# Optimization experiments

Hardware: AMD Instinct MI355X
Metric: run time of the kernel (lower is better)

## Reference

```python
import jax, jax.numpy as jnp
import numpy as np

DIM = 512
D_IN = 4096
N_OBJ = 2048
N_REL = 32768
STEPS = 2
N_OBJ_CLS = 151
N_REL_CLS = 51
EPS = 1e-5


def _mlp2(x, w1, b1, w2, b2):
    # Linear -> ReLU -> Linear (torch Linear: y = x W^T + b)
    return jnp.maximum(x @ w1.T + b1, 0.0) @ w2.T + b2


def _gate(a, b, w, bias):
    # Sequential(Linear(2*dim, 1), Sigmoid) on cat([a, b], 1)
    return jax.nn.sigmoid(jnp.concatenate([a, b], axis=1) @ w.T + bias)


def _gru_cell(x, h, wih, whh, bih, bhh):
    gi = x @ wih.T + bih  # [N, 3*DIM]
    gh = h @ whh.T + bhh
    ir, iz, inew = jnp.split(gi, 3, axis=1)
    hr, hz, hnew = jnp.split(gh, 3, axis=1)
    r = jax.nn.sigmoid(ir + hr)
    z = jax.nn.sigmoid(iz + hz)
    n = jnp.tanh(inew + r * hnew)
    return (1.0 - z) * n + z * h


def setup_inputs() -> dict:
    key = jax.random.key(0)
    ks = jax.random.split(key, 32)
    rn = lambda k, shape, s=0.02: jax.random.normal(k, shape, dtype=jnp.float32) * s
    z = lambda *shape: jnp.zeros(shape, dtype=jnp.float32)
    return {
        'x_obj': jax.random.normal(ks[0], (N_OBJ, D_IN), dtype=jnp.float32),
        'x_pred': jax.random.normal(ks[1], (N_REL, D_IN), dtype=jnp.float32),
        'rel_inds': jax.random.randint(ks[2], (N_REL, 2), 0, N_OBJ),
        # obj / pred embedding MLPs
        'oe_w1': rn(ks[3], (DIM, D_IN)), 'oe_b1': z(DIM),
        'oe_w2': rn(ks[4], (DIM, DIM)), 'oe_b2': z(DIM),
        'pe_w1': rn(ks[5], (DIM, D_IN)), 'pe_b1': z(DIM),
        'pe_w2': rn(ks[6], (DIM, DIM)), 'pe_b2': z(DIM),
        # gates: Linear(2*dim, 1)
        'g_sn_w': rn(ks[7], (1, 2 * DIM)), 'g_sn_b': z(1),
        'g_on_w': rn(ks[8], (1, 2 * DIM)), 'g_on_b': z(1),
        'g_se_w': rn(ks[9], (1, 2 * DIM)), 'g_se_b': z(1),
        'g_oe_w': rn(ks[10], (1, 2 * DIM)), 'g_oe_b': z(1),
        # GRU cells
        'ngru_wih': rn(ks[11], (3 * DIM, DIM)), 'ngru_whh': rn(ks[12], (3 * DIM, DIM)),
        'ngru_bih': z(3 * DIM), 'ngru_bhh': z(3 * DIM),
        'egru_wih': rn(ks[13], (3 * DIM, DIM)), 'egru_whh': rn(ks[14], (3 * DIM, DIM)),
        'egru_bih': z(3 * DIM), 'egru_bhh': z(3 * DIM),
        # classifier heads
        'op_w': rn(ks[15], (N_OBJ_CLS, DIM)), 'op_b': z(N_OBJ_CLS),
        'pp_w': rn(ks[16], (N_REL_CLS, DIM)), 'pp_b': z(N_REL_CLS),
    }


def reference(x_obj, x_pred, rel_inds,
              oe_w1, oe_b1, oe_w2, oe_b2,
              pe_w1, pe_b1, pe_w2, pe_b2,
              g_sn_w, g_sn_b, g_on_w, g_on_b,
              g_se_w, g_se_b, g_oe_w, g_oe_b,
              ngru_wih, ngru_whh, ngru_bih, ngru_bhh,
              egru_wih, egru_whh, egru_bih, egru_bhh,
              op_w, op_b, pp_w, pp_b):
    n_obj = x_obj.shape[0]
    subj_idx = rel_inds[:, 0]
    obj_idx = rel_inds[:, 1]

    h_obj = _mlp2(x_obj, oe_w1, oe_b1, oe_w2, oe_b2)    # [N_obj, DIM]
    h_edge = _mlp2(x_pred, pe_w1, pe_b1, pe_w2, pe_b2)  # [N_rel, DIM]

    # row sums of the 0/1 subj/obj_pred_map == in-degree counts (constants)
    ones = jnp.ones((rel_inds.shape[0],), dtype=jnp.float32)
    cnt_s = jax.ops.segment_sum(ones, subj_idx, num_segments=n_obj)[:, None]
    cnt_o = jax.ops.segment_sum(ones, obj_idx, num_segments=n_obj)[:, None]

    for _ in range(STEPS):
        sub_vert = h_obj[subj_idx]  # [N_rel, DIM]
        obj_vert = h_obj[obj_idx]

        # node update: gated edge->node messages, mean-aggregated per node
        msg_p2s = _gate(sub_vert, h_edge, g_sn_w, g_sn_b) * h_edge
        msg_p2o = _gate(obj_vert, h_edge, g_on_w, g_on_b) * h_edge
        node_message = (
            jax.ops.segment_sum(msg_p2s, subj_idx, num_segments=n_obj) / (cnt_s + EPS)
            + jax.ops.segment_sum(msg_p2o, obj_idx, num_segments=n_obj) / (cnt_o + EPS)
        ) / 2.0
        new_h_obj = _gru_cell(node_message, h_obj, ngru_wih, ngru_whh, ngru_bih, ngru_bhh)

        # edge update: gated node->edge messages
        msg_s2p = _gate(sub_vert, h_edge, g_se_w, g_se_b) * sub_vert
        msg_o2p = _gate(obj_vert, h_edge, g_oe_w, g_oe_b) * obj_vert
        edge_message = (msg_s2p + msg_o2p) / 2.0
        h_edge = _gru_cell(edge_message, h_edge, egru_wih, egru_whh, egru_bih, egru_bhh)
        h_obj = new_h_obj

    obj_class_logits = h_obj @ op_w.T + op_b    # [N_obj, 151]
    pred_class_logits = h_edge @ pp_w.T + pp_b  # [N_rel, 51]
    obj_class_labels = jnp.argmax(obj_class_logits[:, 1:], axis=1) + 1
    return (h_obj, h_edge, obj_class_logits, pred_class_logits, obj_class_labels, rel_inds)
```

## Files before the change

### kernel.cpp

```cpp
#include <hip/hip_runtime.h>
#include <math.h>

typedef unsigned short u16;
typedef unsigned int u32;
typedef _Float16 f16;
typedef f16 f16x8 __attribute__((ext_vector_type(8)));
typedef float f32x4 __attribute__((ext_vector_type(4)));

#define DIM 512
#define D_IN 4096
#define N_OBJS 2048
#define N_RELS 32768
#define N_OBJ_CLS 151
#define N_REL_CLS 51
#define EPSV 1e-5f

#define OFF_HOBJ  0
#define OFF_HEDGE (N_OBJS*DIM)
#define OFF_OLOG  (OFF_HEDGE + N_RELS*DIM)
#define OFF_PLOG  (OFF_OLOG + N_OBJS*N_OBJ_CLS)
#define OFF_LBL   (OFF_PLOG + N_RELS*N_REL_CLS)
#define OFF_RI    (OFF_LBL + N_OBJS)

__device__ __forceinline__ float sigmoidf_(float x) { return 1.0f / (1.0f + expf(-x)); }
__device__ __forceinline__ u16 f2h_(float f) {
    union { f16 h; u16 u; } c; c.h = (f16)f; return c.u;
}
__device__ __forceinline__ float h2f_(u16 u) {
    union { f16 h; u16 u; } c; c.u = u; return (float)c.h;
}

__device__ __forceinline__ void cvt8h1(const float* f, uint4& h) {
    u32 hh[8];
#pragma unroll
    for (int i = 0; i < 8; i++) hh[i] = f2h_(f[i]);
    h.x = hh[0] | (hh[1] << 16); h.y = hh[2] | (hh[3] << 16);
    h.z = hh[4] | (hh[5] << 16); h.w = hh[6] | (hh[7] << 16);
}
__device__ __forceinline__ void cvt8h2(const float* f, uint4& h, uint4& l) {
    u32 hh[8], ll[8];
#pragma unroll
    for (int i = 0; i < 8; i++) {
        u16 x = f2h_(f[i]);
        hh[i] = x;
        ll[i] = f2h_(f[i] - h2f_(x));
    }
    h.x = hh[0] | (hh[1] << 16); h.y = hh[2] | (hh[3] << 16);
    h.z = hh[4] | (hh[5] << 16); h.w = hh[6] | (hh[7] << 16);
    l.x = ll[0] | (ll[1] << 16); l.y = ll[2] | (ll[3] << 16);
    l.z = ll[4] | (ll[5] << 16); l.w = ll[6] | (ll[7] << 16);
}

__device__ __forceinline__ int swzo(int row, int c) {
    return row * 32 + ((c ^ ((row >> 1) & 3)) << 3);
}

__device__ __forceinline__ int xcdswz(int orig, int nwg) {
    const int q = nwg >> 3;
    return (orig & 7) * q + (orig >> 3);
}

__device__ __forceinline__ void gload16(const void* g, void* l) {
    __builtin_amdgcn_global_load_lds(
        (const __attribute__((address_space(1))) void*)g,
        (__attribute__((address_space(3))) void*)l, 16, 0, 0);
}

#define Q_BIG  (DIM * D_IN / 4)
#define Q_SQ   (DIM * DIM / 4)
#define Q_GRU  (3 * DIM * DIM / 4)
#define Q_OP   (N_OBJ_CLS * DIM / 4)
#define Q_PP   (N_REL_CLS * DIM / 4)
#define CV_C0  (Q_BIG)
#define CV_C1  (CV_C0 + Q_BIG)
#define CV_C2  (CV_C1 + Q_SQ)
#define CV_C3  (CV_C2 + Q_SQ)
#define CV_C4  (CV_C3 + Q_GRU)
#define CV_C5  (CV_C4 + Q_GRU)
#define CV_C6  (CV_C5 + Q_GRU)
#define CV_C7  (CV_C6 + Q_GRU)
#define CV_C8  (CV_C7 + Q_OP)
#define CV_C9  (CV_C8 + Q_PP)

__global__ __launch_bounds__(256) void convert_all(
    const float* __restrict__ s0, u16* __restrict__ d0,
    const float* __restrict__ s1, u16* __restrict__ d1,
    const float* __restrict__ s2, u16* __restrict__ d2,
    const float* __restrict__ s3, u16* __restrict__ d3,
    const float* __restrict__ s4, u16* __restrict__ d4,
    const float* __restrict__ s5, u16* __restrict__ d5,
    const float* __restrict__ s6, u16* __restrict__ d6,
    const float* __restrict__ s7, u16* __restrict__ d7,
    const float* __restrict__ s8, u16* __restrict__ d8,
    const float* __restrict__ s9, u16* __restrict__ d9)
{
    int i = blockIdx.x * 256 + threadIdx.x;
    if (i >= CV_C9) return;
    const float* src; u16* dst; int base;
    if      (i < CV_C0) { src = s0; dst = d0; base = 0; }
    else if (i < CV_C1) { src = s1; dst = d1; base = CV_C0; }
    else if (i < CV_C2) { src = s2; dst = d2; base = CV_C1; }
    else if (i < CV_C3) { src = s3; dst = d3; base = CV_C2; }
    else if (i < CV_C4) { src = s4; dst = d4; base = CV_C3; }
    else if (i < CV_C5) { src = s5; dst = d5; base = CV_C4; }
    else if (i < CV_C6) { src = s6; dst = d6; base = CV_C5; }
    else if (i < CV_C7) { src = s7; dst = d7; base = CV_C6; }
    else if (i < CV_C8) { src = s8; dst = d8; base = CV_C7; }
    else                { src = s9; dst = d9; base = CV_C8; }
    const int q = i - base;
    const float4 v = ((const float4*)src)[q];
    ((ushort4*)dst)[q] = make_ushort4(f2h_(v.x), f2h_(v.y), f2h_(v.z), f2h_(v.w));
}

template<bool RELU, int AT, bool WSPLIT>
__device__ __forceinline__ void gemm_a32_body(
    int id, u16* sAh, u16* sBh, u16* sAl,
    const float* __restrict__ A, const u16* __restrict__ Bhi,
    const float* __restrict__ bias, u16* __restrict__ Chi, u16* __restrict__ Clo,
    int NX, int K)
{
    const int m0 = (id / NX) * 128, n0 = (id % NX) * 128;
    const int N = NX * 128;
    const int t = threadIdx.x;
    const int wid = t >> 6, lane = t & 63;
    const int wm = (wid >> 1) * 64, wn = (wid & 1) * 64;
    const int lr = lane & 15, lk = lane >> 4;

    f32x4 acc[4][4] = {};

    const int sr = t >> 1;
    const int sc = (t & 1) * 2;
    const float* Ap = A + (size_t)(m0 + sr) * K + (t & 1) * 16;

    const int rB = (wid * 2) * 16 + (lane >> 2);
    const int cB = (lane & 3) ^ ((rB >> 1) & 3);
    const u16* Bp0 = Bhi + (size_t)(n0 + rB) * K + cB * 8;
    const u16* Bp1 = Bp0 + (size_t)16 * K;
    u16* Bd0 = &sBh[(wid * 2) * 512];
    u16* Bd1 = Bd0 + 512;

    float fv[16];
    *(float4*)&fv[0]  = *(const float4*)(Ap);
    *(float4*)&fv[4]  = *(const float4*)(Ap + 4);
    *(float4*)&fv[8]  = *(const float4*)(Ap + 8);
    *(float4*)&fv[12] = *(const float4*)(Ap + 12);

    for (int k0 = 0; k0 < K; k0 += 32) {
        uint4 ah0, ah1, al0, al1;
        if (AT == 2) { cvt8h2(fv, ah0, al0); cvt8h2(fv + 8, ah1, al1); }
        else         { cvt8h1(fv, ah0);      cvt8h1(fv + 8, ah1); }

        __syncthreads();
        gload16(Bp0 + k0, Bd0);
        gload16(Bp1 + k0, Bd1);
        *(uint4*)&sAh[swzo(sr, sc)]     = ah0;
        *(uint4*)&sAh[swzo(sr, sc + 1)] = ah1;
        if (AT == 2) {
            *(uint4*)&sAl[swzo(sr, sc)]     = al0;
            *(uint4*)&sAl[swzo(sr, sc + 1)] = al1;
        }
        asm volatile("s_waitcnt vmcnt(0)" ::: "memory");
        __syncthreads();

        const int kn = k0 + 32;
        if (kn < K) {
            *(float4*)&fv[0]  = *(const float4*)(Ap + kn);
            *(float4*)&fv[4]  = *(const float4*)(Ap + kn + 4);
            *(float4*)&fv[8]  = *(const float4*)(Ap + kn + 8);
            *(float4*)&fv[12] = *(const float4*)(Ap + kn + 12);
        }

        f16x8 ah[4], al[4], bh[4];
#pragma unroll
        for (int f = 0; f < 4; f++) {
            const int off = swzo(wm + f * 16 + lr, lk);
            ah[f] = *(const f16x8*)&sAh[off];
            if (AT == 2) al[f] = *(const f16x8*)&sAl[off];
            bh[f] = *(const f16x8*)&sBh[swzo(wn + f * 16 + lr, lk)];
        }
#pragma unroll
        for (int fm = 0; fm < 4; fm++)
#pragma unroll
            for (int fn = 0; fn < 4; fn++) {
                acc[fm][fn] = __builtin_amdgcn_mfma_f32_16x16x32_f16(ah[fm], bh[fn], acc[fm][fn], 0, 0, 0);
                if (AT == 2)
                    acc[fm][fn] = __builtin_amdgcn_mfma_f32_16x16x32_f16(al[fm], bh[fn], acc[fm][fn], 0, 0, 0);
            }
    }
#pragma unroll
    for (int fm = 0; fm < 4; fm++) {
        const int mrow = m0 + wm + fm * 16 + lk * 4;
#pragma unroll
        for (int fn = 0; fn < 4; fn++) {
            const int col = n0 + wn + fn * 16 + lr;
            const float bv = bias[col];
#pragma unroll
            for (int j = 0; j < 4; j++) {
                float v = acc[fm][fn][j] + bv;
                if (RELU) v = fmaxf(v, 0.0f);
                const u16 h = f2h_(v);
                Chi[(size_t)(mrow + j) * N + col] = h;
                if (WSPLIT) Clo[(size_t)(mrow + j) * N + col] = f2h_(v - h2f_(h));
            }
        }
    }
}

__global__ __launch_bounds__(256, 3) void enc1_both(
    const float* __restrict__ xp, const u16* __restrict__ pw,
    const float* __restrict__ pb, u16* __restrict__ tmpe,
    const float* __restrict__ xo, const u16* __restrict__ ow,
    const float* __restrict__ ob, u16* __restrict__ tmpoh, u16* __restrict__ tmpol)
{
    __shared__ u16 smem[3 * 4096];
    const int id = xcdswz(blockIdx.x, gridDim.x);
    if (id < 1024)
        gemm_a32_body<true, 1, false>(id, smem, smem + 4096, nullptr,
                                      xp, pw, pb, tmpe, nullptr, 4, D_IN);
    else
        gemm_a32_body<true, 2, true>(id - 1024, smem, smem + 4096, smem + 8192,
                                     xo, ow, ob, tmpoh, tmpol, 4, D_IN);
}

template<int AT, bool WF32, bool WHI, bool WLO>
__device__ __forceinline__ void gemm_f16_body(
    int id, u16* smem,
    const u16* __restrict__ Ahi, const u16* __restrict__ Alo,
    const u16* __restrict__ Bhi, const float* __restrict__ bias,
    float* __restrict__ C32, u16* __restrict__ Chi, u16* __restrict__ Clo,
    int NX, int N, int ldc, int K)
{
    const int m0 = (id / NX) * 128, n0 = (id % NX) * 128;
    const int t = threadIdx.x;
    const int wid = t >> 6, lane = t & 63;
    const int wm = (wid >> 1) * 64, wn = (wid & 1) * 64;
    const int lr = lane & 15, lk = lane >> 4;

    f32x4 acc[4][4] = {};

    const int rr = (wid * 2) * 16 + (lane >> 2);
    const int cc = (lane & 3) ^ ((rr >> 1) & 3);
    const u16* pA0 = Ahi + (size_t)(m0 + rr) * K + cc * 8;
    const u16* pA1 = pA0 + (size_t)16 * K;
    const u16* pL0 = (AT == 2) ? Alo + (size_t)(m0 + rr) * K + cc * 8 : nullptr;
    const u16* pL1 = (AT == 2) ? pL0 + (size_t)16 * K : nullptr;
    const u16* pB0 = Bhi + (size_t)(n0 + rr) * K + cc * 8;
    const u16* pB1 = pB0 + (size_t)16 * K;
    const int bOff = (wid * 2) * 512;

    for (int k0 = 0; k0 < K; k0 += 64) {
        __syncthreads();
#pragma unroll
        for (int h = 0; h < 2; h++) {
            const int kk = k0 + h * 32;
            u16* sA_ = smem + h * 4096;
            u16* sB_ = smem + 8192 + h * 4096;
            gload16(pA0 + kk, sA_ + bOff);
            gload16(pA1 + kk, sA_ + bOff + 512);
            if (AT == 2) {
                u16* sL_ = smem + 16384 + h * 4096;
                gload16(pL0 + kk, sL_ + bOff);
                gload16(pL1 + kk, sL_ + bOff + 512);
            }
            gload16(pB0 + kk, sB_ + bOff);
            gload16(pB1 + kk, sB_ + bOff + 512);
        }
        asm volatile("s_waitcnt vmcnt(0)" ::: "memory");
        __syncthreads();

#pragma unroll
        for (int h = 0; h < 2; h++) {
            const u16* sA_ = smem + h * 4096;
            const u16* sB_ = smem + 8192 + h * 4096;
            const u16* sL_ = smem + 16384 + h * 4096;
            f16x8 ah[4], al[4], bh[4];
#pragma unroll
            for (int f = 0; f < 4; f++) {
                const int off = swzo(wm + f * 16 + lr, lk);
                ah[f] = *(const f16x8*)&sA_[off];
                if (AT == 2) al[f] = *(const f16x8*)&sL_[off];
                bh[f] = *(const f16x8*)&sB_[swzo(wn + f * 16 + lr, lk)];
            }
#pragma unroll
            for (int fm = 0; fm < 4; fm++)
#pragma unroll
                for (int fn = 0; fn < 4; fn++) {
                    acc[fm][fn] = __builtin_amdgcn_mfma_f32_16x16x32_f16(ah[fm], bh[fn], acc[fm][fn], 0, 0, 0);
                    if (AT == 2)
                        acc[fm][fn] = __builtin_amdgcn_mfma_f32_16x16x32_f16(al[fm], bh[fn], acc[fm][fn], 0, 0, 0);
                }
        }
    }
#pragma unroll
    for (int fm = 0; fm < 4; fm++) {
        const int mrow = m0 + wm + fm * 16 + lk * 4;
#pragma unroll
        for (int fn = 0; fn < 4; fn++) {
            const int col = n0 + wn + fn * 16 + lr;
            const float bv = bias[col];
#pragma unroll
            for (int j = 0; j < 4; j++) {
                const float v = acc[fm][fn][j] + bv;
                if (WF32 && col < N) C32[(size_t)(mrow + j) * ldc + col] = v;
                if (WHI) {
                    const u16 h = f2h_(v);
                    Chi[(size_t)(mrow + j) * (NX * 128) + col] = h;
                    if (WLO)
                        Clo[(size_t)(mrow + j) * (NX * 128) + col] = f2h_(v - h2f_(h));
                }
            }
        }
    }
}

template<int AT, bool WF32, bool WHI, bool WLO>
__global__ __launch_bounds__(256, AT == 1 ? 4 : 3) void gemm_f16(
    const u16* __restrict__ Ahi, const u16* __restrict__ Alo,
    const u16* __restrict__ Bhi, const float* __restrict__ bias,
    float* __restrict__ C32, u16* __restrict__ Chi, u16* __restrict__ Clo,
    int NX, int N, int ldc, int K)
{
    __shared__ u16 smem[AT == 2 ? 6 * 4096 : 4 * 4096];
    const int id = xcdswz(blockIdx.x, gridDim.x);
    gemm_f16_body<AT, WF32, WHI, WLO>(id, smem, Ahi, Alo, Bhi, bias,
                                      C32, Chi, Clo, NX, N, ldc, K);
}

__global__ __launch_bounds__(256, 3) void cls_both(
    const u16* __restrict__ hhe, const u16* __restrict__ pph,
    const float* __restrict__ ppb, float* __restrict__ plog,
    const u16* __restrict__ hhoh, const u16* __restrict__ hhol,
    const u16* __restrict__ oph, const float* __restrict__ opb,
    float* __restrict__ olog)
{
    __shared__ u16 smem[6 * 4096];
    const int id = xcdswz(blockIdx.x, gridDim.x);
    if (id < 256)
        gemm_f16_body<1, true, false, false>(id, smem, hhe, nullptr, pph, ppb,
                                             plog, nullptr, nullptr,
                                             1, N_REL_CLS, N_REL_CLS, DIM);
    else
        gemm_f16_body<2, true, false, false>(id - 256, smem, hhoh, hhol, oph, opb,
                                             olog, nullptr, nullptr,
                                             2, N_OBJ_CLS, N_OBJ_CLS, DIM);
}

__global__ __launch_bounds__(256, 4) void gru_gemm_e(
    const u16* __restrict__ Xh, const u16* __restrict__ WiH,
    const float* __restrict__ bi, u16* __restrict__ gi,
    const u16* __restrict__ Hh, const u16* __restrict__ WhH,
    const float* __restrict__ bhs, u16* __restrict__ gh_)
{
    __shared__ u16 smem[4 * 4096];
    const int id = xcdswz(blockIdx.x, gridDim.x);
    const int part = id % 24;
    const int m0b = id / 24;
    const bool isH = part >= 12;
    const int nblk = part - (isH ? 12 : 0);
    gemm_f16_body<1, false, true, false>(m0b * 12 + nblk, smem,
        isH ? Hh : Xh, nullptr, isH ? WhH : WiH, isH ? bhs : bi,
        nullptr, isH ? gh_ : gi, nullptr, 12, 1536, 1536, DIM);
}

__global__ __launch_bounds__(256, 3) void gru_edge_obj(
    const u16* __restrict__ Xe, const u16* __restrict__ WeI,
    const float* __restrict__ beI, u16* __restrict__ geI,
    const u16* __restrict__ He, const u16* __restrict__ WeH,
    const float* __restrict__ beH, u16* __restrict__ geH,
    int nEdge,
    const u16* __restrict__ Xoh, const u16* __restrict__ Xol,
    const u16* __restrict__ WoI, const float* __restrict__ boI, u16* __restrict__ goI,
    const u16* __restrict__ Hoh, const u16* __restrict__ Hol,
    const u16* __restrict__ WoH, const float* __restrict__ boH, u16* __restrict__ goH)
{
    __shared__ u16 smem[6 * 4096];
    const int id = xcdswz(blockIdx.x, gridDim.x);
    if (id < nEdge) {
        const int part = id % 24;
        const int m0b = id / 24;
        const bool isH = part >= 12;
        const int nblk = part - (isH ? 12 : 0);
        gemm_f16_body<1, false, true, false>(m0b * 12 + nblk, smem,
            isH ? He : Xe, nullptr, isH ? WeH : WeI, isH ? beH : beI,
            nullptr, isH ? geH : geI, nullptr, 12, 1536, 1536, DIM);
    } else {
        const int oid = id - nEdge;
        const int part = oid % 24;
        const int m0b = oid / 24;
        const bool isH = part >= 12;
        const int nblk = part - (isH ? 12 : 0);
        gemm_f16_body<2, false, true, false>(m0b * 12 + nblk, smem,
            isH ? Hoh : Xoh, isH ? Hol : Xol, isH ? WoH : WoI, isH ? boH : boI,
            nullptr, isH ? goH : goI, nullptr, 12, 1536, 1536, DIM);
    }
}

__device__ __forceinline__ float gcomb(u16 ir, u16 iz, u16 in_, u16 hr, u16 hz,
                                       u16 hn, float h) {
    const float r = sigmoidf_(h2f_(ir) + h2f_(hr));
    const float z = sigmoidf_(h2f_(iz) + h2f_(hz));
    const float n = tanhf(h2f_(in_) + r * h2f_(hn));
    return (1.0f - z) * n + z * h;
}

template<bool WSPLIT, bool WF32>
__global__ __launch_bounds__(256) void gru_combine(
    const u16* __restrict__ gi, const u16* __restrict__ gh,
    u16* __restrict__ hh, u16* __restrict__ hl, float* __restrict__ H32, int R)
{
    const int idx = blockIdx.x * 256 + threadIdx.x;
    if (idx >= R * 128) return;
    const int r = idx >> 7, c4 = (idx & 127) * 4;
    const size_t gb = (size_t)r * 1536 + c4;
    const ushort4 ir4 = *(const ushort4*)&gi[gb];
    const ushort4 iz4 = *(const ushort4*)&gi[gb + 512];
    const ushort4 in4 = *(const ushort4*)&gi[gb + 1024];
    const ushort4 hr4 = *(const ushort4*)&gh[gb];
    const ushort4 hz4 = *(const ushort4*)&gh[gb + 512];
    const ushort4 hn4 = *(const ushort4*)&gh[gb + 1024];
    const size_t hb = (size_t)r * 512 + c4;
    const ushort4 hhi = *(const ushort4*)&hh[hb];
    float h0 = h2f_(hhi.x), h1 = h2f_(hhi.y), h2 = h2f_(hhi.z), h3 = h2f_(hhi.w);
    if (WSPLIT) {
        const ushort4 hlo = *(const ushort4*)&hl[hb];
        h0 += h2f_(hlo.x); h1 += h2f_(hlo.y); h2 += h2f_(hlo.z); h3 += h2f_(hlo.w);
    }
    float4 o;
    o.x = gcomb(ir4.x, iz4.x, in4.x, hr4.x, hz4.x, hn4.x, h0);
    o.y = gcomb(ir4.y, iz4.y, in4.y, hr4.y, hz4.y, hn4.y, h1);
    o.z = gcomb(ir4.z, iz4.z, in4.z, hr4.z, hz4.z, hn4.z, h2);
    o.w = gcomb(ir4.w, iz4.w, in4.w, hr4.w, hz4.w, hn4.w, h3);
    const ushort4 hi4 = make_ushort4(f2h_(o.x), f2h_(o.y), f2h_(o.z), f2h_(o.w));
    *(ushort4*)&hh[hb] = hi4;
    if (WSPLIT) {
        *(ushort4*)&hl[hb] = make_ushort4(
            f2h_(o.x - h2f_(hi4.x)), f2h_(o.y - h2f_(hi4.y)),
            f2h_(o.z - h2f_(hi4.z)), f2h_(o.w - h2f_(hi4.w)));
    }
    if (WF32) *(float4*)&H32[hb] = o;
}

__global__ __launch_bounds__(256) void count_int(const int* __restrict__ rel,
                                                 int* cs, int* co)
{
    const int e = blockIdx.x * 256 + threadIdx.x;
    atomicAdd(&cs[rel[2 * e]], 1);
    atomicAdd(&co[rel[2 * e + 1]], 1);
}

__global__ __launch_bounds__(256) void scan_off(const int* __restrict__ cs,
    const int* __restrict__ co, int* __restrict__ offs, int* __restrict__ offo)
{
    __shared__ int tmp[256];
    for (int arr = 0; arr < 2; arr++) {
        const int* c = arr ? co : cs;
        int* off = arr ? offo : offs;
        const int base = threadIdx.x * 8;
        int loc[8]; int s = 0;
#pragma unroll
        for (int j = 0; j < 8; j++) { loc[j] = c[base + j]; s += loc[j]; }
        tmp[threadIdx.x] = s;
        __syncthreads();
        for (int d = 1; d < 256; d <<= 1) {
            const int v = (threadIdx.x >= d) ? tmp[threadIdx.x - d] : 0;
            __syncthreads();
            tmp[threadIdx.x] += v;
            __syncthreads();
        }
        int p = tmp[threadIdx.x] - s;
#pragma unroll
        for (int j = 0; j < 8; j++) { off[base + j] = p; p += loc[j]; }
        __syncthreads();
    }
}

__global__ __launch_bounds__(256) void fill_csr(const int* __restrict__ rel,
    int* curS, int* curO, const int* __restrict__ offs, const int* __restrict__ offo,
    int* __restrict__ listS, int* __restrict__ listO)
{
    const int e = blockIdx.x * 256 + threadIdx.x;
    const int s = rel[2 * e], o = rel[2 * e + 1];
    const int i = atomicAdd(&curS[s], 1);
    listS[offs[s] + i] = e;
    const int j = atomicAdd(&curO[o], 1);
    listO[offo[o] + j] = e;
}

__global__ __launch_bounds__(256) void gatepass(
    const u16* __restrict__ hho, const u16* __restrict__ hhe,
    const int* __restrict__ rel,
    const float* __restrict__ wsn, const float* __restrict__ bsn,
    const float* __restrict__ won, const float* __restrict__ bon,
    const float* __restrict__ wse, const float* __restrict__ bse,
    const float* __restrict__ woe, const float* __restrict__ boe,
    const int* __restrict__ cs, const int* __restrict__ co,
    u16* __restrict__ emh, float* __restrict__ af, float* __restrict__ ag)
{
    const int e = blockIdx.x * 4 + (threadIdx.x >> 6);
    const int lane = threadIdx.x & 63;
    const int s = rel[2 * e], o = rel[2 * e + 1];
    const int c = lane * 8;

    const uint4 hsu = *(const uint4*)&hho[(size_t)s * DIM + c];
    const uint4 hou = *(const uint4*)&hho[(size_t)o * DIM + c];
    const uint4 heu = *(const uint4*)&hhe[(size_t)e * DIM + c];
    float hs[8], ho[8], he[8];
    hs[0] = h2f_((u16)hsu.x); hs[1] = h2f_((u16)(hsu.x >> 16));
    hs[2] = h2f_((u16)hsu.y); hs[3] = h2f_((u16)(hsu.y >> 16));
    hs[4] = h2f_((u16)hsu.z); hs[5] = h2f_((u16)(hsu.z >> 16));
    hs[6] = h2f_((u16)hsu.w); hs[7] = h2f_((u16)(hsu.w >> 16));
    ho[0] = h2f_((u16)hou.x); ho[1] = h2f_((u16)(hou.x >> 16));
    ho[2] = h2f_((u16)hou.y); ho[3] = h2f_((u16)(hou.y >> 16));
    ho[4] = h2f_((u16)hou.z); ho[5] = h2f_((u16)(hou.z >> 16));
    ho[6] = h2f_((u16)hou.w); ho[7] = h2f_((u16)(hou.w >> 16));
    he[0] = h2f_((u16)heu.x); he[1] = h2f_((u16)(heu.x >> 16));
    he[2] = h2f_((u16)heu.y); he[3] = h2f_((u16)(heu.y >> 16));
    he[4] = h2f_((u16)heu.z); he[5] = h2f_((u16)(heu.z >> 16));
    he[6] = h2f_((u16)heu.w); he[7] = h2f_((u16)(heu.w >> 16));

    float p0 = 0.f, p1 = 0.f, p2 = 0.f, p3 = 0.f;
#pragma unroll
    for (int q = 0; q < 2; q++) {
        const float4 w0v = *(const float4*)&wsn[c + q * 4];
        const float4 w0e = *(const float4*)&wsn[DIM + c + q * 4];
        const float4 w1v = *(const float4*)&won[c + q * 4];
        const float4 w1e = *(const float4*)&won[DIM + c + q * 4];
        const float4 w2v = *(const float4*)&wse[c + q * 4];
        const float4 w2e = *(const float4*)&wse[DIM + c + q * 4];
        const float4 w3v = *(const float4*)&woe[c + q * 4];
        const float4 w3e = *(const float4*)&woe[DIM + c + q * 4];
        const float* s4 = &hs[q * 4];
        const float* o4 = &ho[q * 4];
        const float* e4 = &he[q * 4];
        p0 += s4[0]*w0v.x + s4[1]*w0v.y + s4[2]*w0v.z + s4[3]*w0v.w
            + e4[0]*w0e.x + e4[1]*w0e.y + e4[2]*w0e.z + e4[3]*w0e.w;
        p1 += o4[0]*w1v.x + o4[1]*w1v.y + o4[2]*w1v.z + o4[3]*w1v.w
            + e4[0]*w1e.x + e4[1]*w1e.y + e4[2]*w1e.z + e4[3]*w1e.w;
        p2 += s4[0]*w2v.x + s4[1]*w2v.y + s4[2]*w2v.z + s4[3]*w2v.w
            + e4[0]*w2e.x + e4[1]*w2e.y + e4[2]*w2e.z + e4[3]*w2e.w;
        p3 += o4[0]*w3v.x + o4[1]*w3v.y + o4[2]*w3v.z + o4[3]*w3v.w
            + e4[0]*w3e.x + e4[1]*w3e.y + e4[2]*w3e.z + e4[3]*w3e.w;
    }
#pragma unroll
    for (int off = 32; off; off >>= 1) {
        p0 += __shfl_xor(p0, off);
        p1 += __shfl_xor(p1, off);
        p2 += __shfl_xor(p2, off);
        p3 += __shfl_xor(p3, off);
    }
    const float gsn = sigmoidf_(p0 + bsn[0]);
    const float gon = sigmoidf_(p1 + bon[0]);
    const float gse = sigmoidf_(p2 + bse[0]);
    const float goe = sigmoidf_(p3 + boe[0]);

    if (lane == 0) {
        af[e] = 0.5f * gsn / ((float)cs[s] + EPSV);
        ag[e] = 0.5f * gon / ((float)co[o] + EPSV);
    }
    u16 em8[8];
#pragma unroll
    for (int j = 0; j < 8; j++)
        em8[j] = f2h_(0.5f * (gse * hs[j] + goe * ho[j]));
    *(uint4*)&emh[(size_t)e * DIM + c] = *(const uint4*)em8;
}

__global__ __launch_bounds__(256) void gather_nm(
    const u16* __restrict__ hhe,
    const int* __restrict__ listS, const int* __restrict__ listO,
    const int* __restrict__ offs, const int* __restrict__ offo,
    const int* __restrict__ cs, const int* __restrict__ co,
    const float* __restrict__ af, const float* __restrict__ ag,
    u16* __restrict__ nmh, u16* __restrict__ nml)
{
    const int v = blockIdx.x * 4 + (threadIdx.x >> 6);
    const int lane = threadIdx.x & 63;
    const int c = lane * 8;

    float acc[8] = {};
#pragma unroll
    for (int side = 0; side < 2; side++) {
        const int* list = side ? listO : listS;
        const int b = side ? offo[v] : offs[v];
        const int n = side ? co[v] : cs[v];
        const float* coef = side ? ag : af;
        for (int i = 0; i < n; i++) {
            const int e = list[b + i];
            const float a = coef[e];
            const uint4 x = *(const uint4*)&hhe[(size_t)e * DIM + c];
            acc[0] += a * h2f_((u16)x.x); acc[1] += a * h2f_((u16)(x.x >> 16));
            acc[2] += a * h2f_((u16)x.y); acc[3] += a * h2f_((u16)(x.y >> 16));
            acc[4] += a * h2f_((u16)x.z); acc[5] += a * h2f_((u16)(x.z >> 16));
            acc[6] += a * h2f_((u16)x.w); acc[7] += a * h2f_((u16)(x.w >> 16));
        }
    }
    u16 hi8[8], lo8[8];
#pragma unroll
    for (int j = 0; j < 8; j++) {
        hi8[j] = f2h_(acc[j]);
        lo8[j] = f2h_(acc[j] - h2f_(hi8[j]));
    }
    *(uint4*)&nmh[(size_t)v * DIM + c] = *(const uint4*)hi8;
    *(uint4*)&nml[(size_t)v * DIM + c] = *(const uint4*)lo8;
}

__global__ __launch_bounds__(256) void argmax_kernel(const float* __restrict__ logits,
                                                     float* __restrict__ out)
{
    const int row = blockIdx.x * 4 + (threadIdx.x >> 6);
    const int lane = threadIdx.x & 63;
    float bv = -1e30f; int bi = 1;
    for (int j = 1 + lane; j < N_OBJ_CLS; j += 64) {
        const float v = logits[(size_t)row * N_OBJ_CLS + j];
        if (v > bv) { bv = v; bi = j; }
    }
#pragma unroll
    for (int off = 32; off; off >>= 1) {
        const float ov = __shfl_xor(bv, off);
        const int oi = __shfl_xor(bi, off);
        if (ov > bv || (ov == bv && oi < bi)) { bv = ov; bi = oi; }
    }
    if (lane == 0) out[row] = (float)bi;
}

__global__ __launch_bounds__(256) void relinds_kernel(const int* __restrict__ rel,
                                                      float* __restrict__ out)
{
    const int i = blockIdx.x * 256 + threadIdx.x;
    out[i] = (float)rel[i];
}

extern "C" void kernel_launch(void* const* d_in, const int* in_sizes, int n_in,
                              void* d_out, int out_size, void* d_ws, size_t ws_size,
                              hipStream_t stream)
{
    const float* x_obj = (const float*)d_in[0];
    const float* x_pred = (const float*)d_in[1];
    const int* rel = (const int*)d_in[2];
    const float* oe_w1 = (const float*)d_in[3];
    const float* oe_b1 = (const float*)d_in[4];
    const float* oe_w2 = (const float*)d_in[5];
    const float* oe_b2 = (const float*)d_in[6];
    const float* pe_w1 = (const float*)d_in[7];
    const float* pe_b1 = (const float*)d_in[8];
    const float* pe_w2 = (const float*)d_in[9];
    const float* pe_b2 = (const float*)d_in[10];
    const float* g_sn_w = (const float*)d_in[11];
    const float* g_sn_b = (const float*)d_in[12];
    const float* g_on_w = (const float*)d_in[13];
    const float* g_on_b = (const float*)d_in[14];
    const float* g_se_w = (const float*)d_in[15];
    const float* g_se_b = (const float*)d_in[16];
    const float* g_oe_w = (const float*)d_in[17];
    const float* g_oe_b = (const float*)d_in[18];
    const float* ngru_wih = (const float*)d_in[19];
    const float* ngru_whh = (const float*)d_in[20];
    const float* ngru_bih = (const float*)d_in[21];
    const float* ngru_bhh = (const float*)d_in[22];
    const float* egru_wih = (const float*)d_in[23];
    const float* egru_whh = (const float*)d_in[24];
    const float* egru_bih = (const float*)d_in[25];
    const float* egru_bhh = (const float*)d_in[26];
    const float* op_w = (const float*)d_in[27];
    const float* op_b = (const float*)d_in[28];
    const float* pp_w = (const float*)d_in[29];
    const float* pp_b = (const float*)d_in[30];

    float* out = (float*)d_out;

    float* h_obj = out + OFF_HOBJ;
    float* h_edge = out + OFF_HEDGE;

    char* wsp = (char*)d_ws;
    float* af = (float*)wsp; wsp += N_RELS * 4;
    float* ag = (float*)wsp; wsp += N_RELS * 4;
    int* cs = (int*)wsp;   wsp += N_OBJS * 4;
    int* co = (int*)wsp;   wsp += N_OBJS * 4;
    int* offs = (int*)wsp; wsp += N_OBJS * 4;
    int* offo = (int*)wsp; wsp += N_OBJS * 4;
    int* curS = (int*)wsp; wsp += N_OBJS * 4;
    int* curO = (int*)wsp; wsp += N_OBJS * 4;
    int* listS = (int*)wsp; wsp += N_RELS * 4;
    int* listO = (int*)wsp; wsp += N_RELS * 4;

    u16* wp = (u16*)wsp;
    const int s_big = DIM * D_IN, s_sq = DIM * DIM, s_gru = 3 * DIM * DIM;
    u16 *oe1h = wp; wp += s_big;
    u16 *pe1h = wp; wp += s_big;
    u16 *oe2h = wp; wp += s_sq;
    u16 *pe2h = wp; wp += s_sq;
    u16 *nih_h = wp; wp += s_gru;
    u16 *nhh_h = wp; wp += s_gru;
    u16 *eih_h = wp; wp += s_gru;
    u16 *ehh_h = wp; wp += s_gru;
    u16 *oph = wp; wp += 256 * DIM;
    u16 *pph = wp; wp += 128 * DIM;
    u16 *tmpo_h = wp; wp += (size_t)N_OBJS * DIM;
    u16 *tmpo_l = wp; wp += (size_t)N_OBJS * DIM;
    u16 *tmpe_h = wp; wp += (size_t)N_RELS * DIM;
    u16 *hhoh = wp; wp += (size_t)N_OBJS * DIM;
    u16 *hhol = wp; wp += (size_t)N_OBJS * DIM;
    u16 *hhe  = wp; wp += (size_t)N_RELS * DIM;
    u16 *emh  = wp; wp += (size_t)N_RELS * DIM;
    u16 *nmh  = wp; wp += (size_t)N_OBJS * DIM;
    u16 *nml  = wp; wp += (size_t)N_OBJS * DIM;
    u16 *gio = wp; wp += (size_t)N_OBJS * 1536;
    u16 *gho = wp; wp += (size_t)N_OBJS * 1536;

    const size_t used = (size_t)((char*)wp - (char*)d_ws);
    int R = 8192;
    if (used + (size_t)16384 * 6144 <= ws_size) R = 16384;
    u16* gi = wp;
    u16* gh = gi + (size_t)R * 1536;

    convert_all<<<(CV_C9 + 255) / 256, 256, 0, stream>>>(
        oe_w1, oe1h, pe_w1, pe1h, oe_w2, oe2h, pe_w2, pe2h,
        ngru_wih, nih_h, ngru_whh, nhh_h, egru_wih, eih_h, egru_whh, ehh_h,
        op_w, oph, pp_w, pph);

    hipMemsetAsync(cs, 0, 2 * N_OBJS * sizeof(int), stream);
    hipMemsetAsync(curS, 0, 2 * N_OBJS * sizeof(int), stream);
    count_int<<<N_RELS / 256, 256, 0, stream>>>(rel, cs, co);
    scan_off<<<1, 256, 0, stream>>>(cs, co, offs, offo);
    fill_csr<<<N_RELS / 256, 256, 0, stream>>>(rel, curS, curO, offs, offo, listS, listO);

    enc1_both<<<1088, 256, 0, stream>>>(
        x_pred, pe1h, pe_b1, tmpe_h,
        x_obj, oe1h, oe_b1, tmpo_h, tmpo_l);
    gemm_f16<1, false, true, false><<<4 * (N_RELS / 128), 256, 0, stream>>>(
        tmpe_h, nullptr, pe2h, pe_b2, nullptr, hhe, nullptr, 4, DIM, DIM, DIM);
    gemm_f16<2, false, true, true><<<4 * (N_OBJS / 128), 256, 0, stream>>>(
        tmpo_h, tmpo_l, oe2h, oe_b2, nullptr, hhoh, hhol, 4, DIM, DIM, DIM);

    for (int step = 0; step < 2; step++) {
        gatepass<<<N_RELS / 4, 256, 0, stream>>>(
            hhoh, hhe, rel,
            g_sn_w, g_sn_b, g_on_w, g_on_b, g_se_w, g_se_b, g_oe_w, g_oe_b,
            cs, co, emh, af, ag);
        gather_nm<<<N_OBJS / 4, 256, 0, stream>>>(
            hhe, listS, listO, offs, offo, cs, co, af, ag, nmh, nml);

        const int Rc0 = (N_RELS < R) ? N_RELS : R;
        const int nEdge = 24 * (Rc0 / 128);
        gru_edge_obj<<<nEdge + 24 * (N_OBJS / 128), 256, 0, stream>>>(
            emh, eih_h, egru_bih, gi, hhe, ehh_h, egru_bhh, gh, nEdge,
            nmh, nml, nih_h, ngru_bih, gio,
            hhoh, hhol, nhh_h, ngru_bhh, gho);

        if (step == 0)
            gru_combine<true, false><<<(N_OBJS * 128 + 255) / 256, 256, 0, stream>>>(
                gio, gho, hhoh, hhol, nullptr, N_OBJS);
        else
            gru_combine<true, true><<<(N_OBJS * 128 + 255) / 256, 256, 0, stream>>>(
                gio, gho, hhoh, hhol, h_obj, N_OBJS);
        if (step == 0)
            gru_combine<false, false><<<(Rc0 * 128 + 255) / 256, 256, 0, stream>>>(
                gi, gh, hhe, nullptr, nullptr, Rc0);
        else
            gru_combine<false, true><<<(Rc0 * 128 + 255) / 256, 256, 0, stream>>>(
                gi, gh, hhe, nullptr, h_edge, Rc0);

        for (int r0 = Rc0; r0 < N_RELS; r0 += R) {
            const int Rc = (N_RELS - r0 < R) ? (N_RELS - r0) : R;
            gru_gemm_e<<<24 * (Rc / 128), 256, 0, stream>>>(
                emh + (size_t)r0 * DIM, eih_h, egru_bih, gi,
                hhe + (size_t)r0 * DIM, ehh_h, egru_bhh, gh);
            if (step == 0)
                gru_combine<false, false><<<(Rc * 128 + 255) / 256, 256, 0, stream>>>(
                    gi, gh, hhe + (size_t)r0 * DIM, nullptr, nullptr, Rc);
            else
                gru_combine<false, true><<<(Rc * 128 + 255) / 256, 256, 0, stream>>>(
                    gi, gh, hhe + (size_t)r0 * DIM, nullptr, h_edge + (size_t)r0 * DIM, Rc);
        }
    }

    cls_both<<<288, 256, 0, stream>>>(
        hhe, pph, pp_b, out + OFF_PLOG,
        hhoh, hhol, oph, op_b, out + OFF_OLOG);

    argmax_kernel<<<N_OBJS / 4, 256, 0, stream>>>(out + OFF_OLOG, out + OFF_LBL);
    relinds_kernel<<<(2 * N_RELS) / 256, 256, 0, stream>>>(rel, out + OFF_RI);
}
```

Before: 1.031 ms.

## Split object GRU GEMM into separate hi/lo passes and fuse rel_inds output

The object-side GRU GEMM previously used a two-operand (hi+lo) split-precision body. It now runs as two independent single-operand GEMMs, one on the hi part and one on the lo part with a zero bias, writing separate hi/lo gate buffers. A new combine kernel sums these in fp32. This gives the combined edge+object kernel a uniform, lighter body, so it drops to 4-wave occupancy and a smaller shared-memory footprint. The rel_inds float copy moves into fill_csr, removing one launch. The cost is extra gate buffers and the memory traffic for them.

Result: faster. 982.3 us (median of 2 runs) (-4.7%).

```diff
diff --git a/kernel.cpp b/kernel.cpp
--- a/kernel.cpp
+++ b/kernel.cpp
@@ -362,18 +362,21 @@
         nullptr, isH ? gh_ : gi, nullptr, 12, 1536, 1536, DIM);
 }
 
-__global__ __launch_bounds__(256, 3) void gru_edge_obj(
+__global__ __launch_bounds__(256, 4) void gru_all1(
     const u16* __restrict__ Xe, const u16* __restrict__ WeI,
     const float* __restrict__ beI, u16* __restrict__ geI,
     const u16* __restrict__ He, const u16* __restrict__ WeH,
     const float* __restrict__ beH, u16* __restrict__ geH,
     int nEdge,
     const u16* __restrict__ Xoh, const u16* __restrict__ Xol,
-    const u16* __restrict__ WoI, const float* __restrict__ boI, u16* __restrict__ goI,
     const u16* __restrict__ Hoh, const u16* __restrict__ Hol,
-    const u16* __restrict__ WoH, const float* __restrict__ boH, u16* __restrict__ goH)
-{
-    __shared__ u16 smem[6 * 4096];
+    const u16* __restrict__ WoI, const u16* __restrict__ WoH,
+    const float* __restrict__ boI, const float* __restrict__ boH,
+    const float* __restrict__ zb,
+    u16* __restrict__ gioh, u16* __restrict__ giol,
+    u16* __restrict__ ghoh, u16* __restrict__ ghol)
+{
+    __shared__ u16 smem[4 * 4096];
     const int id = xcdswz(blockIdx.x, gridDim.x);
     if (id < nEdge) {
         const int part = id % 24;
@@ -383,30 +386,39 @@
         gemm_f16_body<1, false, true, false>(m0b * 12 + nblk, smem,
             isH ? He : Xe, nullptr, isH ? WeH : WeI, isH ? beH : beI,
             nullptr, isH ? geH : geI, nullptr, 12, 1536, 1536, DIM);
-    } else {
+    } else if (id < nEdge + 384) {
         const int oid = id - nEdge;
         const int part = oid % 24;
         const int m0b = oid / 24;
         const bool isH = part >= 12;
         const int nblk = part - (isH ? 12 : 0);
-        gemm_f16_body<2, false, true, false>(m0b * 12 + nblk, smem,
-            isH ? Hoh : Xoh, isH ? Hol : Xol, isH ? WoH : WoI, isH ? boH : boI,
-            nullptr, isH ? goH : goI, nullptr, 12, 1536, 1536, DIM);
-    }
-}
-
-__device__ __forceinline__ float gcomb(u16 ir, u16 iz, u16 in_, u16 hr, u16 hz,
-                                       u16 hn, float h) {
-    const float r = sigmoidf_(h2f_(ir) + h2f_(hr));
-    const float z = sigmoidf_(h2f_(iz) + h2f_(hz));
-    const float n = tanhf(h2f_(in_) + r * h2f_(hn));
+        gemm_f16_body<1, false, true, false>(m0b * 12 + nblk, smem,
+            isH ? Hoh : Xoh, nullptr, isH ? WoH : WoI, isH ? boH : boI,
+            nullptr, isH ? ghoh : gioh, nullptr, 12, 1536, 1536, DIM);
+    } else {
+        const int oid = id - nEdge - 384;
+        const int part = oid % 24;
+        const int m0b = oid / 24;
+        const bool isH = part >= 12;
+        const int nblk = part - (isH ? 12 : 0);
+        gemm_f16_body<1, false, true, false>(m0b * 12 + nblk, smem,
+            isH ? Hol : Xol, nullptr, isH ? WoH : WoI, zb,
+            nullptr, isH ? ghol : giol, nullptr, 12, 1536, 1536, DIM);
+    }
+}
+
+__device__ __forceinline__ float gcomb(float ir, float iz, float in_,
+                                       float hr, float hz, float hn, float h) {
+    const float r = sigmoidf_(ir + hr);
+    const float z = sigmoidf_(iz + hz);
+    const float n = tanhf(in_ + r * hn);
     return (1.0f - z) * n + z * h;
 }
 
-template<bool WSPLIT, bool WF32>
+template<bool WF32>
 __global__ __launch_bounds__(256) void gru_combine(
     const u16* __restrict__ gi, const u16* __restrict__ gh,
-    u16* __restrict__ hh, u16* __restrict__ hl, float* __restrict__ H32, int R)
+    u16* __restrict__ hh, float* __restrict__ H32, int R)
 {
     const int idx = blockIdx.x * 256 + threadIdx.x;
     if (idx >= R * 128) return;
@@ -420,24 +432,68 @@
     const ushort4 hn4 = *(const ushort4*)&gh[gb + 1024];
     const size_t hb = (size_t)r * 512 + c4;
     const ushort4 hhi = *(const ushort4*)&hh[hb];
-    float h0 = h2f_(hhi.x), h1 = h2f_(hhi.y), h2 = h2f_(hhi.z), h3 = h2f_(hhi.w);
-    if (WSPLIT) {
-        const ushort4 hlo = *(const ushort4*)&hl[hb];
-        h0 += h2f_(hlo.x); h1 += h2f_(hlo.y); h2 += h2f_(hlo.z); h3 += h2f_(hlo.w);
-    }
     float4 o;
-    o.x = gcomb(ir4.x, iz4.x, in4.x, hr4.x, hz4.x, hn4.x, h0);
-    o.y = gcomb(ir4.y, iz4.y, in4.y, hr4.y, hz4.y, hn4.y, h1);
-    o.z = gcomb(ir4.z, iz4.z, in4.z, hr4.z, hz4.z, hn4.z, h2);
-    o.w = gcomb(ir4.w, iz4.w, in4.w, hr4.w, hz4.w, hn4.w, h3);
-    const ushort4 hi4 = make_ushort4(f2h_(o.x), f2h_(o.y), f2h_(o.z), f2h_(o.w));
+    o.x = gcomb(h2f_(ir4.x), h2f_(iz4.x), h2f_(in4.x),
+                h2f_(hr4.x), h2f_(hz4.x), h2f_(hn4.x), h2f_(hhi.x));
+    o.y = gcomb(h2f_(ir4.y), h2f_(iz4.y), h2f_(in4.y),
+                h2f_(hr4.y), h2f_(hz4.y), h2f_(hn4.y), h2f_(hhi.y));
+    o.z = gcomb(h2f_(ir4.z), h2f_(iz4.z), h2f_(in4.z),
+                h2f_(hr4.z), h2f_(hz4.z), h2f_(hn4.z), h2f_(hhi.z));
+    o.w = gcomb(h2f_(ir4.w), h2f_(iz4.w), h2f_(in4.w),
+                h2f_(hr4.w), h2f_(hz4.w), h2f_(hn4.w), h2f_(hhi.w));
+    *(ushort4*)&hh[hb] = make_ushort4(f2h_(o.x), f2h_(o.y), f2h_(o.z), f2h_(o.w));
+    if (WF32) *(float4*)&H32[hb] = o;
+}
+
+template<bool WF32>
+__global__ __launch_bounds__(256) void gru_combine_o2(
+    const u16* __restrict__ gih, const u16* __restrict__ gil,
+    const u16* __restrict__ ghh_, const u16* __restrict__ ghl_,
+    u16* __restrict__ hh, u16* __restrict__ hl, float* __restrict__ H32, int R)
+{
+    const int idx = blockIdx.x * 256 + threadIdx.x;
+    if (idx >= R * 128) return;
+    const int r = idx >> 7, c4 = (idx & 127) * 4;
+    const size_t gb = (size_t)r * 1536 + c4;
+    ushort4 a, b;
+    float ir[4], iz[4], in_[4], hr[4], hz[4], hn[4];
+    a = *(const ushort4*)&gih[gb];        b = *(const ushort4*)&gil[gb];
+    ir[0] = h2f_(a.x) + h2f_(b.x); ir[1] = h2f_(a.y) + h2f_(b.y);
+    ir[2] = h2f_(a.z) + h2f_(b.z); ir[3] = h2f_(a.w) + h2f_(b.w);
+    a = *(const ushort4*)&gih[gb + 512];  b = *(const ushort4*)&gil[gb + 512];
+    iz[0] = h2f_(a.x) + h2f_(b.x); iz[1] = h2f_(a.y) + h2f_(b.y);
+    iz[2] = h2f_(a.z) + h2f_(b.z); iz[3] = h2f_(a.w) + h2f_(b.w);
+    a = *(const ushort4*)&gih[gb + 1024]; b = *(const ushort4*)&gil[gb + 1024];
+    in_[0] = h2f_(a.x) + h2f_(b.x); in_[1] = h2f_(a.y) + h2f_(b.y);
+    in_[2] = h2f_(a.z) + h2f_(b.z); in_[3] = h2f_(a.w) + h2f_(b.w);
+    a = *(const ushort4*)&ghh_[gb];        b = *(const ushort4*)&ghl_[gb];
+    hr[0] = h2f_(a.x) + h2f_(b.x); hr[1] = h2f_(a.y) + h2f_(b.y);
+    hr[2] = h2f_(a.z) + h2f_(b.z); hr[3] = h2f_(a.w) + h2f_(b.w);
+    a = *(const ushort4*)&ghh_[gb + 512];  b = *(const ushort4*)&ghl_[gb + 512];
+    hz[0] = h2f_(a.x) + h2f_(b.x); hz[1] = h2f_(a.y) + h2f_(b.y);
+    hz[2] = h2f_(a.z) + h2f_(b.z); hz[3] = h2f_(a.w) + h2f_(b.w);
+    a = *(const ushort4*)&ghh_[gb + 1024]; b = *(const ushort4*)&ghl_[gb + 1024];
+    hn[0] = h2f_(a.x) + h2f_(b.x); hn[1] = h2f_(a.y) + h2f_(b.y);
+    hn[2] = h2f_(a.z) + h2f_(b.z); hn[3] = h2f_(a.w) + h2f_(b.w);
+
+    const size_t hb = (size_t)r * 512 + c4;
+    const ushort4 hhi = *(const ushort4*)&hh[hb];
+    const ushort4 hlo = *(const ushort4*)&hl[hb];
+    float h[4];
+    h[0] = h2f_(hhi.x) + h2f_(hlo.x); h[1] = h2f_(hhi.y) + h2f_(hlo.y);
+    h[2] = h2f_(hhi.z) + h2f_(hlo.z); h[3] = h2f_(hhi.w) + h2f_(hlo.w);
+
+    float o[4];
+#pragma unroll
+    for (int j = 0; j < 4; j++)
+        o[j] = gcomb(ir[j], iz[j], in_[j], hr[j], hz[j], hn[j], h[j]);
+
+    const ushort4 hi4 = make_ushort4(f2h_(o[0]), f2h_(o[1]), f2h_(o[2]), f2h_(o[3]));
     *(ushort4*)&hh[hb] = hi4;
-    if (WSPLIT) {
-        *(ushort4*)&hl[hb] = make_ushort4(
-            f2h_(o.x - h2f_(hi4.x)), f2h_(o.y - h2f_(hi4.y)),
-            f2h_(o.z - h2f_(hi4.z)), f2h_(o.w - h2f_(hi4.w)));
-    }
-    if (WF32) *(float4*)&H32[hb] = o;
+    *(ushort4*)&hl[hb] = make_ushort4(
+        f2h_(o[0] - h2f_(hi4.x)), f2h_(o[1] - h2f_(hi4.y)),
+        f2h_(o[2] - h2f_(hi4.z)), f2h_(o[3] - h2f_(hi4.w)));
+    if (WF32) *(float4*)&H32[hb] = make_float4(o[0], o[1], o[2], o[3]);
 }
 
 __global__ __launch_bounds__(256) void count_int(const int* __restrict__ rel,
@@ -476,7 +532,7 @@
 
 __global__ __launch_bounds__(256) void fill_csr(const int* __restrict__ rel,
     int* curS, int* curO, const int* __restrict__ offs, const int* __restrict__ offo,
-    int* __restrict__ listS, int* __restrict__ listO)
+    int* __restrict__ listS, int* __restrict__ listO, float* __restrict__ outri)
 {
     const int e = blockIdx.x * 256 + threadIdx.x;
     const int s = rel[2 * e], o = rel[2 * e + 1];
@@ -484,6 +540,8 @@
     listS[offs[s] + i] = e;
     const int j = atomicAdd(&curO[o], 1);
     listO[offo[o] + j] = e;
+    outri[2 * e]     = (float)s;
+    outri[2 * e + 1] = (float)o;
 }
 
 __global__ __launch_bounds__(256) void gatepass(
@@ -620,13 +678,6 @@
         if (ov > bv || (ov == bv && oi < bi)) { bv = ov; bi = oi; }
     }
     if (lane == 0) out[row] = (float)bi;
-}
-
-__global__ __launch_bounds__(256) void relinds_kernel(const int* __restrict__ rel,
-                                                      float* __restrict__ out)
-{
-    const int i = blockIdx.x * 256 + threadIdx.x;
-    out[i] = (float)rel[i];
 }
 
 extern "C" void kernel_launch(void* const* d_in, const int* in_sizes, int n_in,
@@ -673,6 +724,7 @@
     char* wsp = (char*)d_ws;
     float* af = (float*)wsp; wsp += N_RELS * 4;
     float* ag = (float*)wsp; wsp += N_RELS * 4;
+    float* zbias = (float*)wsp; wsp += 1536 * 4;
     int* cs = (int*)wsp;   wsp += N_OBJS * 4;
     int* co = (int*)wsp;   wsp += N_OBJS * 4;
     int* offs = (int*)wsp; wsp += N_OBJS * 4;
@@ -703,8 +755,10 @@
     u16 *emh  = wp; wp += (size_t)N_RELS * DIM;
     u16 *nmh  = wp; wp += (size_t)N_OBJS * DIM;
     u16 *nml  = wp; wp += (size_t)N_OBJS * DIM;
-    u16 *gio = wp; wp += (size_t)N_OBJS * 1536;
-    u16 *gho = wp; wp += (size_t)N_OBJS * 1536;
+    u16 *gioh = wp; wp += (size_t)N_OBJS * 1536;
+    u16 *giol = wp; wp += (size_t)N_OBJS * 1536;
+    u16 *ghoh = wp; wp += (size_t)N_OBJS * 1536;
+    u16 *ghol = wp; wp += (size_t)N_OBJS * 1536;
 
     const size_t used = (size_t)((char*)wp - (char*)d_ws);
     int R = 8192;
@@ -719,9 +773,11 @@
 
     hipMemsetAsync(cs, 0, 2 * N_OBJS * sizeof(int), stream);
     hipMemsetAsync(curS, 0, 2 * N_OBJS * sizeof(int), stream);
+    hipMemsetAsync(zbias, 0, 1536 * sizeof(float), stream);
     count_int<<<N_RELS / 256, 256, 0, stream>>>(rel, cs, co);
     scan_off<<<1, 256, 0, stream>>>(cs, co, offs, offo);
-    fill_csr<<<N_RELS / 256, 256, 0, stream>>>(rel, curS, curO, offs, offo, listS, listO);
+    fill_csr<<<N_RELS / 256, 256, 0, stream>>>(rel, curS, curO, offs, offo,
+                                               listS, listO, out + OFF_RI);
 
     enc1_both<<<1088, 256, 0, stream>>>(
         x_pred, pe1h, pe_b1, tmpe_h,
@@ -741,23 +797,23 @@
 
         const int Rc0 = (N_RELS < R) ? N_RELS : R;
         const int nEdge = 24 * (Rc0 / 128);
-        gru_edge_obj<<<nEdge + 24 * (N_OBJS / 128), 256, 0, stream>>>(
+        gru_all1<<<nEdge + 768, 256, 0, stream>>>(
             emh, eih_h, egru_bih, gi, hhe, ehh_h, egru_bhh, gh, nEdge,
-            nmh, nml, nih_h, ngru_bih, gio,
-            hhoh, hhol, nhh_h, ngru_bhh, gho);
+            nmh, nml, hhoh, hhol, nih_h, nhh_h, ngru_bih, ngru_bhh, zbias,
+            gioh, giol, ghoh, ghol);
 
         if (step == 0)
-            gru_combine<true, false><<<(N_OBJS * 128 + 255) / 256, 256, 0, stream>>>(
-                gio, gho, hhoh, hhol, nullptr, N_OBJS);
+            gru_combine_o2<false><<<(N_OBJS * 128 + 255) / 256, 256, 0, stream>>>(
+                gioh, giol, ghoh, ghol, hhoh, hhol, nullptr, N_OBJS);
         else
-            gru_combine<true, true><<<(N_OBJS * 128 + 255) / 256, 256, 0, stream>>>(
-                gio, gho, hhoh, hhol, h_obj, N_OBJS);
+            gru_combine_o2<true><<<(N_OBJS * 128 + 255) / 256, 256, 0, stream>>>(
+                gioh, giol, ghoh, ghol, hhoh, hhol, h_obj, N_OBJS);
         if (step == 0)
-            gru_combine<false, false><<<(Rc0 * 128 + 255) / 256, 256, 0, stream>>>(
-                gi, gh, hhe, nullptr, nullptr, Rc0);
+            gru_combine<false><<<(Rc0 * 128 + 255) / 256, 256, 0, stream>>>(
+                gi, gh, hhe, nullptr, Rc0);
         else
-            gru_combine<false, true><<<(Rc0 * 128 + 255) / 256, 256, 0, stream>>>(
-                gi, gh, hhe, nullptr, h_edge, Rc0);
+            gru_combine<true><<<(Rc0 * 128 + 255) / 256, 256, 0, stream>>>(
+                gi, gh, hhe, h_edge, Rc0);
 
         for (int r0 = Rc0; r0 < N_RELS; r0 += R) {
             const int Rc = (N_RELS - r0 < R) ? (N_RELS - r0) : R;
@@ -765,11 +821,11 @@
                 emh + (size_t)r0 * DIM, eih_h, egru_bih, gi,
                 hhe + (size_t)r0 * DIM, ehh_h, egru_bhh, gh);
             if (step == 0)
-                gru_combine<false, false><<<(Rc * 128 + 255) / 256, 256, 0, stream>>>(
-                    gi, gh, hhe + (size_t)r0 * DIM, nullptr, nullptr, Rc);
+                gru_combine<false><<<(Rc * 128 + 255) / 256, 256, 0, stream>>>(
+                    gi, gh, hhe + (size_t)r0 * DIM, nullptr, Rc);
             else
-                gru_combine<false, true><<<(Rc * 128 + 255) / 256, 256, 0, stream>>>(
-                    gi, gh, hhe + (size_t)r0 * DIM, nullptr, h_edge + (size_t)r0 * DIM, Rc);
+                gru_combine<true><<<(Rc * 128 + 255) / 256, 256, 0, stream>>>(
+                    gi, gh, hhe + (size_t)r0 * DIM, h_edge + (size_t)r0 * DIM, Rc);
         }
     }
 
@@ -778,5 +834,4 @@
         hhoh, hhol, oph, op_b, out + OFF_OLOG);
 
     argmax_kernel<<<N_OBJS / 4, 256, 0, stream>>>(out + OFF_OLOG, out + OFF_LBL);
-    relinds_kernel<<<(2 * N_RELS) / 256, 256, 0, stream>>>(rel, out + OFF_RI);
-}
+}
```
